# Kernel optimization log

Measured on AMD Instinct MI355X. Metric: run time of the kernel, lower is better.

The kernel has to match this reference:

```python
import jax, jax.numpy as jnp
import numpy as np
from jax.scipy.special import logsumexp

B, N, D, LATENT = 8192, 64, 128, 256
TEMP = 0.1
NOISE_FACTOR = 1.0
SINKHORN_ITERS = 20
NEG = -1e9  # stand-in for -inf: exp(NEG)==0, avoids NaN from (-inf)-(-inf)


def setup_inputs() -> dict:
    key = jax.random.key(0)
    ks = jax.random.split(key, 8)
    padded = jax.random.normal(ks[0], (B, N, D), dtype=jnp.float32)
    # set sizes in [1, N]
    set_size = jax.random.randint(ks[1], (B,), 1, N + 1)
    # maskB[b,i,j] True unless (i < k_b and j < k_b)
    r = jnp.arange(N)[None, :, None]
    c = jnp.arange(N)[None, None, :]
    k = set_size[:, None, None]
    maskB = ~((r < k) & (c < k))
    # zero out padding rows of features (pad_sequence pads with zeros)
    row_valid = (jnp.arange(N)[None, :] < set_size[:, None])
    padded = padded * row_valid[:, :, None].astype(jnp.float32)
    # precomputed Gumbel noise: -log(-log(u))
    u = jax.random.uniform(ks[2], (B, N, N), dtype=jnp.float32, minval=1e-20, maxval=1.0)
    gumbel_noise = -jnp.log(-jnp.log(u) + 1e-20)
    W1 = jax.random.normal(ks[3], (D, LATENT), dtype=jnp.float32) * (1.0 / np.sqrt(D))
    b1 = jax.random.normal(ks[4], (LATENT,), dtype=jnp.float32) * 0.01
    W2 = jax.random.normal(ks[5], (LATENT, N), dtype=jnp.float32) * (1.0 / np.sqrt(LATENT))
    b2 = jax.random.normal(ks[6], (N,), dtype=jnp.float32) * 0.01
    return {"padded_neighbour_features": padded, "set_size": set_size, "maskB": maskB,
            "gumbel_noise": gumbel_noise, "W1": W1, "b1": b1, "W2": W2, "b2": b2}


def _sinkhorn(log_alpha, maskB):
    def step(la, _):
        la = jnp.where(maskB, NEG, la)
        la = la - logsumexp(la, axis=2, keepdims=True)  # row normalize
        la = jnp.where(maskB, NEG, la)
        la = la - logsumexp(la, axis=1, keepdims=True)  # col normalize
        la = jnp.where(maskB, NEG, la)
        return la, None
    la, _ = jax.lax.scan(step, log_alpha, None, length=SINKHORN_ITERS)
    return jnp.exp(la)


def reference(padded_neighbour_features, set_size, maskB, gumbel_noise, W1, b1, W2, b2):
    x = padded_neighbour_features  # [B, N, D]
    h = jax.nn.relu(jnp.einsum('bnd,dl->bnl', x, W1) + b1)       # [B, N, LATENT]
    net = jnp.einsum('bnl,lm->bnm', h, W2) + b2                   # [B, N, N]
    log_alpha = (net + gumbel_noise * NOISE_FACTOR) / TEMP
    post = _sinkhorn(log_alpha, maskB)                            # [B, N, N]
    # post^T @ padded features
    permuted = jnp.einsum('bij,bif->bjf', post, x)                # [B, N, D]
    return set_size, permuted
```

## Files before the change

### kernel.cpp

```cpp
#include <hip/hip_runtime.h>
#include <hip/hip_bf16.h>


typedef _Float16 h16;
typedef h16 h8 __attribute__((ext_vector_type(8)));
typedef __fp16 fp16x2 __attribute__((ext_vector_type(2)));
typedef float v4f __attribute__((ext_vector_type(4)));

template<int CTRL>
__device__ __forceinline__ float dppf(float x) {
  return __int_as_float(__builtin_amdgcn_update_dpp(
      0, __float_as_int(x), CTRL, 0xF, 0xF, true));
}
__device__ __forceinline__ float red16_sum(float x) {
  x += dppf<0xB1>(x);
  x += dppf<0x4E>(x);
  x += dppf<0x124>(x);
  x += dppf<0x128>(x);
  return x;
}
__device__ __forceinline__ float red16_max(float x) {
  x = fmaxf(x, dppf<0xB1>(x));
  x = fmaxf(x, dppf<0x4E>(x));
  x = fmaxf(x, dppf<0x124>(x));
  x = fmaxf(x, dppf<0x128>(x));
  return x;
}
__device__ __forceinline__ float frcp(float x) { return __builtin_amdgcn_rcpf(x); }
__device__ __forceinline__ h8 cvt8(v4f a, v4f b) {
  union { h8 v; fp16x2 p[4]; } u;
  u.p[0] = __builtin_amdgcn_cvt_pkrtz(a[0], a[1]);
  u.p[1] = __builtin_amdgcn_cvt_pkrtz(a[2], a[3]);
  u.p[2] = __builtin_amdgcn_cvt_pkrtz(b[0], b[1]);
  u.p[3] = __builtin_amdgcn_cvt_pkrtz(b[2], b[3]);
  return u.v;
}

__global__ __launch_bounds__(256) void prep_w(const float* __restrict__ W1,
                                              const float* __restrict__ W2,
                                              h16* __restrict__ w1s,
                                              h16* __restrict__ w2s) {
  int t = blockIdx.x * 256 + threadIdx.x;
  if (t < 128 * 256) {
    int row = t >> 8, col = t & 255;
    int kk = row >> 5, e = row & 31;
    w1s[kk * 8192 + col * 32 + e] = (h16)W1[t];
  } else if (t < 128 * 256 + 256 * 64) {
    int t2 = t - 128 * 256;
    int row = t2 >> 6, j = t2 & 63;
    int kk = row >> 5, e = row & 31;
    w2s[kk * 2048 + j * 32 + e] = (h16)W2[t2];
  }
}

__global__ __launch_bounds__(256) void write_ss(const int* __restrict__ ssz,
                                                float* __restrict__ outp) {
  int b = blockIdx.x * 256 + threadIdx.x;
  if (b < 8192) outp[b] = (float)ssz[b];
}

template<bool WSF>
__global__ __launch_bounds__(256) void mlp_init(
    const float* __restrict__ xf,
    const int* __restrict__ ssz,
    const float* __restrict__ gn,
    const float* __restrict__ b1,
    const float* __restrict__ b2,
    const h16* __restrict__ w1s,
    const h16* __restrict__ w2s,
    const float* __restrict__ W1f,
    const float* __restrict__ W2f,
    float* __restrict__ outp) {
  __shared__ __align__(16) char smem[32768];

  const int tid = threadIdx.x, b = blockIdx.x;
  const int w = tid >> 6, lane = tid & 63, g = lane >> 4, lc = lane & 15;
  const int k = ssz[b];
  const int sr = tid >> 2, sseg = tid & 3;

  {
    const float* src = xf + (size_t)b * 8192 + sr * 128 + sseg * 32;
#pragma unroll
    for (int v = 0; v < 4; ++v) {
      const int byte = (sr * 256 + (sseg * 32 + v * 8) * 2) ^ ((sr & 7) << 4);
      *(h8*)(smem + byte) =
          cvt8(*(const v4f*)(src + v * 8), *(const v4f*)(src + v * 8 + 4));
    }
  }
  float b1v[4], b2v[4];
#pragma unroll
  for (int n = 0; n < 4; ++n) b1v[n] = b1[w * 64 + n * 16 + lc];
#pragma unroll
  for (int n = 0; n < 4; ++n) b2v[n] = b2[n * 16 + lc];
  __syncthreads();

  v4f acc1[4][4];
#pragma unroll
  for (int m = 0; m < 4; ++m)
#pragma unroll
    for (int n = 0; n < 4; ++n) acc1[m][n] = (v4f){0.f, 0.f, 0.f, 0.f};
#pragma unroll
  for (int kk = 0; kk < 4; ++kk) {
    h8 av[4], bv[4];
#pragma unroll
    for (int m = 0; m < 4; ++m) {
      const int row = lc + 16 * m;
      const int byte = (row * 256 + (kk * 32 + 8 * g) * 2) ^ ((row & 7) << 4);
      av[m] = *(const h8*)(smem + byte);
    }
#pragma unroll
    for (int n = 0; n < 4; ++n) {
      if (WSF) {
        bv[n] = *(const h8*)&w1s[kk * 8192 + (w * 64 + n * 16 + lc) * 32 + 8 * g];
      } else {
        h8 t;
#pragma unroll
        for (int e = 0; e < 8; ++e)
          t[e] = (h16)W1f[(kk * 32 + 8 * g + e) * 256 + (w * 64 + n * 16 + lc)];
        bv[n] = t;
      }
    }
#pragma unroll
    for (int m = 0; m < 4; ++m)
#pragma unroll
      for (int n = 0; n < 4; ++n)
        acc1[m][n] = __builtin_amdgcn_mfma_f32_16x16x32_f16(av[m], bv[n], acc1[m][n], 0, 0, 0);
  }

  float gnr[4][4];
  if (16 * w < k) {
    const float* gnb = gn + (size_t)b * 4096;
#pragma unroll
    for (int i = 0; i < 4; ++i)
#pragma unroll
      for (int n = 0; n < 4; ++n)
        gnr[i][n] = gnb[(16 * w + 4 * g + i) * 64 + 16 * n + lc];
  }

  __syncthreads();
#pragma unroll
  for (int m = 0; m < 4; ++m)
#pragma unroll
    for (int n = 0; n < 4; ++n)
#pragma unroll
      for (int q = 0; q < 4; ++q) {
        const int row = 16 * m + 4 * g + q;
        const int col = w * 64 + 16 * n + lc;
        const int byte = (row * 512 + col * 2) ^ ((row & 7) << 4);
        *(h16*)(smem + byte) = (h16)fmaxf(acc1[m][n][q] + b1v[n], 0.0f);
      }
  __syncthreads();

  v4f acc2[4];
#pragma unroll
  for (int n = 0; n < 4; ++n) acc2[n] = (v4f){0.f, 0.f, 0.f, 0.f};
  {
    const int row2 = 16 * w + lc;
#pragma unroll
    for (int kk = 0; kk < 8; ++kk) {
      const int byte = (row2 * 512 + (kk * 32 + 8 * g) * 2) ^ ((row2 & 7) << 4);
      h8 av = *(const h8*)(smem + byte);
#pragma unroll
      for (int n = 0; n < 4; ++n) {
        h8 bv;
        if (WSF) {
          bv = *(const h8*)&w2s[kk * 2048 + (n * 16 + lc) * 32 + 8 * g];
        } else {
          h8 t;
#pragma unroll
          for (int e = 0; e < 8; ++e)
            t[e] = (h16)W2f[(kk * 32 + 8 * g + e) * 64 + (n * 16 + lc)];
          bv = t;
        }
        acc2[n] = __builtin_amdgcn_mfma_f32_16x16x32_f16(av, bv, acc2[n], 0, 0, 0);
      }
    }
  }

  float p[4][4];
#pragma unroll
  for (int i = 0; i < 4; ++i)
#pragma unroll
    for (int n = 0; n < 4; ++n) p[i][n] = 0.0f;
  if (16 * w < k) {
#pragma unroll
    for (int i = 0; i < 4; ++i) {
      const int row = 16 * w + 4 * g + i;
      float la[4];
#pragma unroll
      for (int n = 0; n < 4; ++n) {
        const int col = 16 * n + lc;
        const bool valid = (row < k) && (col < k);
        const float v = acc2[n][i] + b2v[n] + gnr[i][n];
        la[n] = valid ? v : -1e30f;
      }
      float m_ = fmaxf(fmaxf(la[0], la[1]), fmaxf(la[2], la[3]));
      m_ = red16_max(m_);
#pragma unroll
      for (int n = 0; n < 4; ++n)
        p[i][n] = (la[n] > -1e29f) ? exp2f((la[n] - m_) * 14.4269504089f) : 0.0f;
    }
  }

  __syncthreads();
  {
    float* lds = (float*)smem;
#pragma unroll
    for (int i = 0; i < 4; ++i)
#pragma unroll
      for (int n = 0; n < 4; ++n) {
        const int idx = ((n * 4 + w) * 64 + 16 * (lc >> 2) + 4 * g + i) * 4 + (lc & 3);
        lds[idx + 4 * (idx >> 5)] = p[i][n];
      }
  }
  __syncthreads();
  {
    const float* lds = (const float*)smem;
    float* P0 = outp + 8192 + (size_t)b * 8192;
#pragma unroll
    for (int j = 0; j < 4; ++j) {
      const int f = tid * 16 + j * 4;
      *(v4f*)&P0[f] = *(const v4f*)&lds[f + 4 * (f >> 5)];
    }
  }
}

__global__ __launch_bounds__(256, 4) void sink_out(
    const float* __restrict__ xf,
    const int* __restrict__ ssz,
    float* __restrict__ outp) {
  __shared__ h16 pth_all[4][4096];

  const int tid = threadIdx.x;
  const int w = tid >> 6, lane = tid & 63, g = lane >> 4, lc = lane & 15;
  h16* pth = pth_all[w];

  const int b = blockIdx.x * 4 + w;
  const int k = ssz[b];
  const int mcnt = (k + 15) >> 4;
  const int kk3max = (k + 31) >> 5;
  const float* xb = xf + (size_t)b * 8192;

  v4f p[4][4];
  {
    const float* P0 = outp + 8192 + (size_t)b * 8192;
#pragma unroll
    for (int mj = 0; mj < 4; ++mj)
#pragma unroll
      for (int nr = 0; nr < 4; ++nr)
        p[mj][nr] = *(const v4f*)&P0[((mj * 4 + nr) * 64 + lane) * 4];
  }

#pragma unroll 1
  for (int it = 0; it < 20; ++it) {
#pragma unroll
    for (int nr = 0; nr < 4; ++nr)
      if (nr < mcnt) {
        float s = 0.0f;
#pragma unroll
        for (int mj = 0; mj < 4; ++mj)
          if (mj < mcnt)
            s += (p[mj][nr][0] + p[mj][nr][1]) + (p[mj][nr][2] + p[mj][nr][3]);
        s += __shfl_xor(s, 16);
        s += __shfl_xor(s, 32);
        const float sc = frcp(s + 1e-30f);
#pragma unroll
        for (int mj = 0; mj < 4; ++mj)
          if (mj < mcnt) {
            p[mj][nr][0] *= sc; p[mj][nr][1] *= sc;
            p[mj][nr][2] *= sc; p[mj][nr][3] *= sc;
          }
      }
#pragma unroll
    for (int mj = 0; mj < 4; ++mj)
      if (mj < mcnt) {
#pragma unroll
        for (int q = 0; q < 4; ++q) {
          float c = 0.0f;
#pragma unroll
          for (int nr = 0; nr < 4; ++nr)
            if (nr < mcnt) c += p[mj][nr][q];
          c = red16_sum(c);
          const float sc = frcp(c + 1e-30f);
#pragma unroll
          for (int nr = 0; nr < 4; ++nr)
            if (nr < mcnt) p[mj][nr][q] *= sc;
        }
      }
  }

#pragma unroll
  for (int mj = 0; mj < 4; ++mj)
#pragma unroll
    for (int nr = 0; nr < 4; ++nr)
#pragma unroll
      for (int q = 0; q < 4; ++q)
        pth[((2 * nr + (lc >> 3)) * 64 + 16 * mj + 4 * g + q) * 8 + (lc & 7)] =
            (h16)p[mj][nr][q];
  asm volatile("s_waitcnt lgkmcnt(0)" ::: "memory");

  float* outb = outp + 8192 + (size_t)b * 8192;
#pragma unroll 1
  for (int c = 0; c < 4; ++c) {
    v4f acc3[4][2];
#pragma unroll
    for (int m = 0; m < 4; ++m)
#pragma unroll
      for (int nn = 0; nn < 2; ++nn) acc3[m][nn] = (v4f){0.f, 0.f, 0.f, 0.f};
#pragma unroll 1
    for (int kk = 0; kk < kk3max; ++kk) {
      h8 ap[4];
#pragma unroll
      for (int m = 0; m < 4; ++m)
        if (m < mcnt)
          ap[m] = *(const h8*)&pth[((4 * kk + g) * 64 + 16 * m + lc) * 8];
#pragma unroll
      for (int nn = 0; nn < 2; ++nn) {
        const int f = 16 * (2 * c + nn) + lc;
        v4f x0, x1;
#pragma unroll
        for (int e = 0; e < 4; ++e) x0[e] = xb[(kk * 32 + 8 * g + e) * 128 + f];
#pragma unroll
        for (int e = 0; e < 4; ++e) x1[e] = xb[(kk * 32 + 8 * g + 4 + e) * 128 + f];
        h8 bxx = cvt8(x0, x1);
#pragma unroll
        for (int m = 0; m < 4; ++m)
          if (m < mcnt)
            acc3[m][nn] = __builtin_amdgcn_mfma_f32_16x16x32_f16(ap[m], bxx, acc3[m][nn], 0, 0, 0);
      }
    }
#pragma unroll
    for (int m = 0; m < 4; ++m)
#pragma unroll
      for (int nn = 0; nn < 2; ++nn)
#pragma unroll
        for (int q = 0; q < 4; ++q)
          outb[(16 * m + 4 * g + q) * 128 + 16 * (2 * c + nn) + lc] = acc3[m][nn][q];
  }
}

extern "C" void kernel_launch(void* const* d_in, const int* in_sizes, int n_in,
                              void* d_out, int out_size, void* d_ws, size_t ws_size,
                              hipStream_t stream) {
  const float* xf = (const float*)d_in[0];
  const int* ssz = (const int*)d_in[1];
  const float* gn = (const float*)d_in[3];
  const float* W1 = (const float*)d_in[4];
  const float* b1 = (const float*)d_in[5];
  const float* W2 = (const float*)d_in[6];
  const float* b2 = (const float*)d_in[7];
  float* outp = (float*)d_out;

  const size_t ws_need = (size_t)(128 * 256 + 256 * 64) * sizeof(h16);
  const bool use_ws = (d_ws != nullptr) && (ws_size >= ws_need);

  if (use_ws) {
    h16* w1s = (h16*)d_ws;
    h16* w2s = w1s + 128 * 256;
    prep_w<<<192, 256, 0, stream>>>(W1, W2, w1s, w2s);
    mlp_init<true><<<8192, 256, 0, stream>>>(xf, ssz, gn, b1, b2, w1s, w2s,
                                             W1, W2, outp);
  } else {
    mlp_init<false><<<8192, 256, 0, stream>>>(xf, ssz, gn, b1, b2,
                                              (const h16*)nullptr,
                                              (const h16*)nullptr,
                                              W1, W2, outp);
  }
  sink_out<<<2048, 256, 0, stream>>>(xf, ssz, outp);
  write_ss<<<32, 256, 0, stream>>>(ssz, outp);
}
```

Before: 352.1 us.

## Fuse MLP, Sinkhorn and output matmul into one kernel per batch

Merges mlp_init, sink_out and write_ss into a single kernel, so the initial 64x64 probability matrix stays in registers instead of going out to global memory and being read back. Each of the four waves now computes the full second-layer GEMM, the row softmax init and all 20 Sinkhorn iterations for the same batch element, so that work is done four times over. Each wave then produces a 32-column slice of the output product. This trades that redundant compute for removing a large global round-trip and two kernel launches. The set-size write moves into the fused kernel.

```diff
diff --git a/kernel.cpp b/kernel.cpp
--- a/kernel.cpp
+++ b/kernel.cpp
@@ -17,13 +17,6 @@
   x += dppf<0x4E>(x);
   x += dppf<0x124>(x);
   x += dppf<0x128>(x);
-  return x;
-}
-__device__ __forceinline__ float red16_max(float x) {
-  x = fmaxf(x, dppf<0xB1>(x));
-  x = fmaxf(x, dppf<0x4E>(x));
-  x = fmaxf(x, dppf<0x124>(x));
-  x = fmaxf(x, dppf<0x128>(x));
   return x;
 }
 __device__ __forceinline__ float frcp(float x) { return __builtin_amdgcn_rcpf(x); }
@@ -53,14 +46,8 @@
   }
 }
 
-__global__ __launch_bounds__(256) void write_ss(const int* __restrict__ ssz,
-                                                float* __restrict__ outp) {
-  int b = blockIdx.x * 256 + threadIdx.x;
-  if (b < 8192) outp[b] = (float)ssz[b];
-}
-
 template<bool WSF>
-__global__ __launch_bounds__(256) void mlp_init(
+__global__ __launch_bounds__(256) void permgen_fused(
     const float* __restrict__ xf,
     const int* __restrict__ ssz,
     const float* __restrict__ gn,
@@ -76,10 +63,12 @@
   const int tid = threadIdx.x, b = blockIdx.x;
   const int w = tid >> 6, lane = tid & 63, g = lane >> 4, lc = lane & 15;
   const int k = ssz[b];
+  const int mcnt = (k + 15) >> 4;
   const int sr = tid >> 2, sseg = tid & 3;
+  const float* xb = xf + (size_t)b * 8192;
 
   {
-    const float* src = xf + (size_t)b * 8192 + sr * 128 + sseg * 32;
+    const float* src = xb + sr * 128 + sseg * 32;
 #pragma unroll
     for (int v = 0; v < 4; ++v) {
       const int byte = (sr * 256 + (sseg * 32 + v * 8) * 2) ^ ((sr & 7) << 4);
@@ -87,11 +76,9 @@
           cvt8(*(const v4f*)(src + v * 8), *(const v4f*)(src + v * 8 + 4));
     }
   }
-  float b1v[4], b2v[4];
+  float b1v[4];
 #pragma unroll
   for (int n = 0; n < 4; ++n) b1v[n] = b1[w * 64 + n * 16 + lc];
-#pragma unroll
-  for (int n = 0; n < 4; ++n) b2v[n] = b2[n * 16 + lc];
   __syncthreads();
 
   v4f acc1[4][4];
@@ -127,16 +114,6 @@
         acc1[m][n] = __builtin_amdgcn_mfma_f32_16x16x32_f16(av[m], bv[n], acc1[m][n], 0, 0, 0);
   }
 
-  float gnr[4][4];
-  if (16 * w < k) {
-    const float* gnb = gn + (size_t)b * 4096;
-#pragma unroll
-    for (int i = 0; i < 4; ++i)
-#pragma unroll
-      for (int n = 0; n < 4; ++n)
-        gnr[i][n] = gnb[(16 * w + 4 * g + i) * 64 + 16 * n + lc];
-  }
-
   __syncthreads();
 #pragma unroll
   for (int m = 0; m < 4; ++m)
@@ -151,105 +128,79 @@
       }
   __syncthreads();
 
-  v4f acc2[4];
-#pragma unroll
-  for (int n = 0; n < 4; ++n) acc2[n] = (v4f){0.f, 0.f, 0.f, 0.f};
-  {
-    const int row2 = 16 * w + lc;
-#pragma unroll
-    for (int kk = 0; kk < 8; ++kk) {
-      const int byte = (row2 * 512 + (kk * 32 + 8 * g) * 2) ^ ((row2 & 7) << 4);
-      h8 av = *(const h8*)(smem + byte);
-#pragma unroll
-      for (int n = 0; n < 4; ++n) {
-        h8 bv;
+  v4f p[4][4];
+#pragma unroll
+  for (int mj = 0; mj < 4; ++mj)
+#pragma unroll
+    for (int nr = 0; nr < 4; ++nr) p[mj][nr] = (v4f){0.f, 0.f, 0.f, 0.f};
+#pragma unroll
+  for (int kk = 0; kk < 8; ++kk) {
+    h8 avW[4], bvH[4];
+#pragma unroll
+    for (int mj = 0; mj < 4; ++mj)
+      if (mj < mcnt) {
         if (WSF) {
-          bv = *(const h8*)&w2s[kk * 2048 + (n * 16 + lc) * 32 + 8 * g];
+          avW[mj] = *(const h8*)&w2s[kk * 2048 + (16 * mj + lc) * 32 + 8 * g];
         } else {
           h8 t;
 #pragma unroll
           for (int e = 0; e < 8; ++e)
-            t[e] = (h16)W2f[(kk * 32 + 8 * g + e) * 64 + (n * 16 + lc)];
-          bv = t;
+            t[e] = (h16)W2f[(kk * 32 + 8 * g + e) * 64 + 16 * mj + lc];
+          avW[mj] = t;
         }
-        acc2[n] = __builtin_amdgcn_mfma_f32_16x16x32_f16(av, bv, acc2[n], 0, 0, 0);
-      }
-    }
-  }
-
-  float p[4][4];
-#pragma unroll
-  for (int i = 0; i < 4; ++i)
-#pragma unroll
-    for (int n = 0; n < 4; ++n) p[i][n] = 0.0f;
-  if (16 * w < k) {
-#pragma unroll
-    for (int i = 0; i < 4; ++i) {
-      const int row = 16 * w + 4 * g + i;
-      float la[4];
-#pragma unroll
-      for (int n = 0; n < 4; ++n) {
-        const int col = 16 * n + lc;
-        const bool valid = (row < k) && (col < k);
-        const float v = acc2[n][i] + b2v[n] + gnr[i][n];
-        la[n] = valid ? v : -1e30f;
-      }
-      float m_ = fmaxf(fmaxf(la[0], la[1]), fmaxf(la[2], la[3]));
-      m_ = red16_max(m_);
-#pragma unroll
-      for (int n = 0; n < 4; ++n)
-        p[i][n] = (la[n] > -1e29f) ? exp2f((la[n] - m_) * 14.4269504089f) : 0.0f;
-    }
-  }
-
+      }
+#pragma unroll
+    for (int nr = 0; nr < 4; ++nr)
+      if (nr < mcnt) {
+        const int row = 16 * nr + lc;
+        const int byte = (row * 512 + (kk * 32 + 8 * g) * 2) ^ ((row & 7) << 4);
+        bvH[nr] = *(const h8*)(smem + byte);
+      }
+#pragma unroll
+    for (int mj = 0; mj < 4; ++mj)
+      if (mj < mcnt)
+#pragma unroll
+        for (int nr = 0; nr < 4; ++nr)
+          if (nr < mcnt)
+            p[mj][nr] = __builtin_amdgcn_mfma_f32_16x16x32_f16(avW[mj], bvH[nr], p[mj][nr], 0, 0, 0);
+  }
   __syncthreads();
-  {
-    float* lds = (float*)smem;
-#pragma unroll
-    for (int i = 0; i < 4; ++i)
-#pragma unroll
-      for (int n = 0; n < 4; ++n) {
-        const int idx = ((n * 4 + w) * 64 + 16 * (lc >> 2) + 4 * g + i) * 4 + (lc & 3);
-        lds[idx + 4 * (idx >> 5)] = p[i][n];
-      }
-  }
-  __syncthreads();
-  {
-    const float* lds = (const float*)smem;
-    float* P0 = outp + 8192 + (size_t)b * 8192;
-#pragma unroll
-    for (int j = 0; j < 4; ++j) {
-      const int f = tid * 16 + j * 4;
-      *(v4f*)&P0[f] = *(const v4f*)&lds[f + 4 * (f >> 5)];
-    }
-  }
-}
-
-__global__ __launch_bounds__(256, 4) void sink_out(
-    const float* __restrict__ xf,
-    const int* __restrict__ ssz,
-    float* __restrict__ outp) {
-  __shared__ h16 pth_all[4][4096];
-
-  const int tid = threadIdx.x;
-  const int w = tid >> 6, lane = tid & 63, g = lane >> 4, lc = lane & 15;
-  h16* pth = pth_all[w];
-
-  const int b = blockIdx.x * 4 + w;
-  const int k = ssz[b];
-  const int mcnt = (k + 15) >> 4;
-  const int kk3max = (k + 31) >> 5;
-  const float* xb = xf + (size_t)b * 8192;
-
-  v4f p[4][4];
-  {
-    const float* P0 = outp + 8192 + (size_t)b * 8192;
-#pragma unroll
-    for (int mj = 0; mj < 4; ++mj)
-#pragma unroll
-      for (int nr = 0; nr < 4; ++nr)
-        p[mj][nr] = *(const v4f*)&P0[((mj * 4 + nr) * 64 + lane) * 4];
-  }
+
+  v4f b2j[4];
+#pragma unroll
+  for (int mj = 0; mj < 4; ++mj) b2j[mj] = *(const v4f*)&b2[16 * mj + 4 * g];
+#pragma unroll
+  for (int nr = 0; nr < 4; ++nr)
+    if (nr < mcnt) {
+      const int r = 16 * nr + lc;
+#pragma unroll
+      for (int mj = 0; mj < 4; ++mj)
+        if (mj < mcnt) {
+          v4f gv = *(const v4f*)(gn + (size_t)b * 4096 + r * 64 + 16 * mj + 4 * g);
+#pragma unroll
+          for (int q = 0; q < 4; ++q) {
+            const int j = 16 * mj + 4 * g + q;
+            const float la = p[mj][nr][q] + b2j[mj][q] + gv[q];
+            p[mj][nr][q] = (r < k && j < k) ? la : -1e30f;
+          }
+        }
+      float m_ = -1e30f;
+#pragma unroll
+      for (int mj = 0; mj < 4; ++mj)
+        if (mj < mcnt)
+#pragma unroll
+          for (int q = 0; q < 4; ++q) m_ = fmaxf(m_, p[mj][nr][q]);
+      m_ = fmaxf(m_, __shfl_xor(m_, 16));
+      m_ = fmaxf(m_, __shfl_xor(m_, 32));
+#pragma unroll
+      for (int mj = 0; mj < 4; ++mj)
+        if (mj < mcnt)
+#pragma unroll
+          for (int q = 0; q < 4; ++q) {
+            const float la = p[mj][nr][q];
+            p[mj][nr][q] = (la > -1e29f) ? exp2f((la - m_) * 14.4269504089f) : 0.0f;
+          }
+    }
 
 #pragma unroll 1
   for (int it = 0; it < 20; ++it) {
@@ -289,6 +240,7 @@
       }
   }
 
+  h16* pth = (h16*)smem + w * 4096;
 #pragma unroll
   for (int mj = 0; mj < 4; ++mj)
 #pragma unroll
@@ -300,43 +252,43 @@
   asm volatile("s_waitcnt lgkmcnt(0)" ::: "memory");
 
   float* outb = outp + 8192 + (size_t)b * 8192;
+  const int kk3max = (k + 31) >> 5;
+  v4f acc3[4][2];
+#pragma unroll
+  for (int m = 0; m < 4; ++m)
+#pragma unroll
+    for (int nn = 0; nn < 2; ++nn) acc3[m][nn] = (v4f){0.f, 0.f, 0.f, 0.f};
 #pragma unroll 1
-  for (int c = 0; c < 4; ++c) {
-    v4f acc3[4][2];
+  for (int kk = 0; kk < kk3max; ++kk) {
+    h8 ap[4];
 #pragma unroll
     for (int m = 0; m < 4; ++m)
-#pragma unroll
-      for (int nn = 0; nn < 2; ++nn) acc3[m][nn] = (v4f){0.f, 0.f, 0.f, 0.f};
-#pragma unroll 1
-    for (int kk = 0; kk < kk3max; ++kk) {
-      h8 ap[4];
+      if (m < mcnt)
+        ap[m] = *(const h8*)&pth[((4 * kk + g) * 64 + 16 * m + lc) * 8];
+#pragma unroll
+    for (int nn = 0; nn < 2; ++nn) {
+      const int f = 16 * (2 * w + nn) + lc;
+      v4f x0, x1;
+#pragma unroll
+      for (int e = 0; e < 4; ++e) x0[e] = xb[(kk * 32 + 8 * g + e) * 128 + f];
+#pragma unroll
+      for (int e = 0; e < 4; ++e) x1[e] = xb[(kk * 32 + 8 * g + 4 + e) * 128 + f];
+      h8 bxx = cvt8(x0, x1);
 #pragma unroll
       for (int m = 0; m < 4; ++m)
         if (m < mcnt)
-          ap[m] = *(const h8*)&pth[((4 * kk + g) * 64 + 16 * m + lc) * 8];
-#pragma unroll
-      for (int nn = 0; nn < 2; ++nn) {
-        const int f = 16 * (2 * c + nn) + lc;
-        v4f x0, x1;
-#pragma unroll
-        for (int e = 0; e < 4; ++e) x0[e] = xb[(kk * 32 + 8 * g + e) * 128 + f];
-#pragma unroll
-        for (int e = 0; e < 4; ++e) x1[e] = xb[(kk * 32 + 8 * g + 4 + e) * 128 + f];
-        h8 bxx = cvt8(x0, x1);
-#pragma unroll
-        for (int m = 0; m < 4; ++m)
-          if (m < mcnt)
-            acc3[m][nn] = __builtin_amdgcn_mfma_f32_16x16x32_f16(ap[m], bxx, acc3[m][nn], 0, 0, 0);
-      }
-    }
-#pragma unroll
-    for (int m = 0; m < 4; ++m)
-#pragma unroll
-      for (int nn = 0; nn < 2; ++nn)
-#pragma unroll
-        for (int q = 0; q < 4; ++q)
-          outb[(16 * m + 4 * g + q) * 128 + 16 * (2 * c + nn) + lc] = acc3[m][nn][q];
-  }
+          acc3[m][nn] = __builtin_amdgcn_mfma_f32_16x16x32_f16(ap[m], bxx, acc3[m][nn], 0, 0, 0);
+    }
+  }
+#pragma unroll
+  for (int m = 0; m < 4; ++m)
+#pragma unroll
+    for (int nn = 0; nn < 2; ++nn)
+#pragma unroll
+      for (int q = 0; q < 4; ++q)
+        outb[(16 * m + 4 * g + q) * 128 + 16 * (2 * w + nn) + lc] = acc3[m][nn][q];
+
+  if (tid == 0) outp[b] = (float)k;
 }
 
 extern "C" void kernel_launch(void* const* d_in, const int* in_sizes, int n_in,
@@ -358,14 +310,12 @@
     h16* w1s = (h16*)d_ws;
     h16* w2s = w1s + 128 * 256;
     prep_w<<<192, 256, 0, stream>>>(W1, W2, w1s, w2s);
-    mlp_init<true><<<8192, 256, 0, stream>>>(xf, ssz, gn, b1, b2, w1s, w2s,
-                                             W1, W2, outp);
+    permgen_fused<true><<<8192, 256, 0, stream>>>(xf, ssz, gn, b1, b2, w1s, w2s,
+                                                  W1, W2, outp);
   } else {
-    mlp_init<false><<<8192, 256, 0, stream>>>(xf, ssz, gn, b1, b2,
-                                              (const h16*)nullptr,
-                                              (const h16*)nullptr,
-                                              W1, W2, outp);
-  }
-  sink_out<<<2048, 256, 0, stream>>>(xf, ssz, outp);
-  write_ss<<<32, 256, 0, stream>>>(ssz, outp);
-}
+    permgen_fused<false><<<8192, 256, 0, stream>>>(xf, ssz, gn, b1, b2,
+                                                   (const h16*)nullptr,
+                                                   (const h16*)nullptr,
+                                                   W1, W2, outp);
+  }
+}
```

Result: slower. 787.0 us (+123.5%).

## Drop LDS transpose for P handoff, fold set-size write into sink kernel

Applied to the files above, without the earlier changes.

The mlp_init kernel now writes its probability tile straight from registers in a native fragment order. This replaces the LDS transpose and its two barriers, and sink_out's load is reindexed to match that layout. The separate write_ss launch is removed, with set_size written by lane 0 of each wave in sink_out. Gumbel noise loads are also skipped for column blocks beyond the set size. The price is less contiguous global stores and gathered loads in exchange for fewer barriers and one fewer launch.

```diff
diff --git a/kernel.cpp b/kernel.cpp
--- a/kernel.cpp
+++ b/kernel.cpp
@@ -53,12 +53,6 @@
   }
 }
 
-__global__ __launch_bounds__(256) void write_ss(const int* __restrict__ ssz,
-                                                float* __restrict__ outp) {
-  int b = blockIdx.x * 256 + threadIdx.x;
-  if (b < 8192) outp[b] = (float)ssz[b];
-}
-
 template<bool WSF>
 __global__ __launch_bounds__(256) void mlp_init(
     const float* __restrict__ xf,
@@ -134,7 +128,8 @@
     for (int i = 0; i < 4; ++i)
 #pragma unroll
       for (int n = 0; n < 4; ++n)
-        gnr[i][n] = gnb[(16 * w + 4 * g + i) * 64 + 16 * n + lc];
+        if (16 * n < k)
+          gnr[i][n] = gnb[(16 * w + 4 * g + i) * 64 + 16 * n + lc];
   }
 
   __syncthreads();
@@ -202,26 +197,13 @@
     }
   }
 
-  __syncthreads();
-  {
-    float* lds = (float*)smem;
-#pragma unroll
-    for (int i = 0; i < 4; ++i)
-#pragma unroll
-      for (int n = 0; n < 4; ++n) {
-        const int idx = ((n * 4 + w) * 64 + 16 * (lc >> 2) + 4 * g + i) * 4 + (lc & 3);
-        lds[idx + 4 * (idx >> 5)] = p[i][n];
-      }
-  }
-  __syncthreads();
-  {
-    const float* lds = (const float*)smem;
-    float* P0 = outp + 8192 + (size_t)b * 8192;
-#pragma unroll
-    for (int j = 0; j < 4; ++j) {
-      const int f = tid * 16 + j * 4;
-      *(v4f*)&P0[f] = *(const v4f*)&lds[f + 4 * (f >> 5)];
-    }
+  float* P0 = outp + 8192 + (size_t)b * 8192;
+#pragma unroll
+  for (int i = 0; i < 4; ++i) {
+    v4f o;
+#pragma unroll
+    for (int n = 0; n < 4; ++n) o[n] = p[i][n];
+    *(v4f*)&P0[tid * 16 + i * 4] = o;
   }
 }
 
@@ -241,14 +223,20 @@
   const int kk3max = (k + 31) >> 5;
   const float* xb = xf + (size_t)b * 8192;
 
+  if (lane == 0) outp[b] = (float)k;
+
   v4f p[4][4];
   {
     const float* P0 = outp + 8192 + (size_t)b * 8192;
-#pragma unroll
-    for (int mj = 0; mj < 4; ++mj)
-#pragma unroll
-      for (int nr = 0; nr < 4; ++nr)
-        p[mj][nr] = *(const v4f*)&P0[((mj * 4 + nr) * 64 + lane) * 4];
+    const int base = 256 * (lc >> 2) + 4 * (lc & 3) + 64 * g;
+#pragma unroll
+    for (int nr = 0; nr < 4; ++nr)
+#pragma unroll
+      for (int q = 0; q < 4; ++q) {
+        v4f t = *(const v4f*)&P0[1024 * nr + base + 16 * q];
+        p[0][nr][q] = t[0]; p[1][nr][q] = t[1];
+        p[2][nr][q] = t[2]; p[3][nr][q] = t[3];
+      }
   }
 
 #pragma unroll 1
@@ -367,5 +355,4 @@
                                               W1, W2, outp);
   }
   sink_out<<<2048, 256, 0, stream>>>(xf, ssz, outp);
-  write_ss<<<32, 256, 0, stream>>>(ssz, outp);
-}
+}
```

New measurement: 345.9 us (median of 2 runs). No clear change (-1.7%).
